# Optimization experiments

Measured on AMD Instinct MI355X. Metric: run time of the kernel, lower is better.

The kernel has to match this reference:

```python
import jax, jax.numpy as jnp
import numpy as np

B, N_FEAT, SEQ, E, H, V = 32, 196, 64, 1024, 1024, 32000


def setup_inputs() -> dict:
    key = jax.random.key(0)
    ks = jax.random.split(key, 16)
    s = 0.02
    return {
        "features": jax.random.normal(ks[0], (B, N_FEAT, E), jnp.float32),
        "captions": jax.random.randint(ks[1], (B, SEQ), 0, V),
        "max_seq_length": SEQ,
        # decoder embedding table (vocab, embed)
        "emb": jax.random.normal(ks[2], (V, E), jnp.float32) * s,
        # attention MLP: Linear(E->H), Tanh, Linear(H->1)
        "Wa1": jax.random.normal(ks[3], (H, E), jnp.float32) * s,
        "ba1": jnp.zeros((H,), jnp.float32),
        "Wa2": jax.random.normal(ks[4], (1, H), jnp.float32) * s,
        "ba2": jnp.zeros((1,), jnp.float32),
        # GRU (1 layer), input = concat(word_emb, context) -> E + H
        "W_ih": jax.random.normal(ks[5], (3 * H, E + H), jnp.float32) * s,
        "W_hh": jax.random.normal(ks[6], (3 * H, H), jnp.float32) * s,
        "b_ih": jnp.zeros((3 * H,), jnp.float32),
        "b_hh": jnp.zeros((3 * H,), jnp.float32),
        # output projection Linear(H -> V)
        "W_fc": jax.random.normal(ks[7], (V, H), jnp.float32) * s,
        "b_fc": jnp.zeros((V,), jnp.float32),
    }


def reference(features, captions, max_seq_length, emb, Wa1, ba1, Wa2, ba2,
              W_ih, W_hh, b_ih, b_hh, W_fc, b_fc):
    # words: (B, S, E)
    words = emb[captions]
    # combined: (B, N_FEAT + S, E)
    combined = jnp.concatenate([features, words], axis=1)
    # attention scores over the combined tokens, softmax along token axis
    scores = jnp.tanh(combined @ Wa1.T + ba1) @ Wa2.T + ba2   # (B, M, 1)
    A = jax.nn.softmax(scores, axis=1)                         # (B, M, 1)
    # context h0 = A^T @ combined -> (B, E); used both as GRU h0 and per-step context
    h0 = jnp.sum(A * combined, axis=1)
    context = h0

    def gru_cell(x, h):
        gi = x @ W_ih.T + b_ih          # (B, 3H)
        gh = h @ W_hh.T + b_hh          # (B, 3H)
        ir, iz, inn = jnp.split(gi, 3, axis=-1)
        hr, hz, hn = jnp.split(gh, 3, axis=-1)
        r = jax.nn.sigmoid(ir + hr)
        z = jax.nn.sigmoid(iz + hz)
        n = jnp.tanh(inn + r * hn)
        return (1.0 - z) * n + z * h

    def step(carry, _):
        input_word, h = carry
        x = jnp.concatenate([emb[input_word], context], axis=-1)  # (B, E+H)
        h_new = gru_cell(x, h)
        out = h_new @ W_fc.T + b_fc                               # (B, V)
        # greedy feedback (eval path / no teacher forcing)
        next_word = jnp.argmax(out, axis=-1)
        return (next_word, h_new), out

    init = (captions[:, 0], h0)
    (_, _), outs = jax.lax.scan(step, init, None, length=max_seq_length - 1)
    outs = jnp.transpose(outs, (1, 0, 2))                         # (B, S-1, V)
    bsz = captions.shape[0]
    vocab = W_fc.shape[0]
    outputs = jnp.concatenate(
        [jnp.zeros((bsz, 1, vocab), outs.dtype), outs], axis=1)   # t=0 stays zero
    return outputs, A
```

## Files before the change

kernel.cpp:

```cpp
#include <hip/hip_runtime.h>
#include <hip/hip_bf16.h>

typedef unsigned long long ull;
typedef unsigned int uint;

#define NB 32
#define NFEAT 196
#define SEQL 64
#define ED 1024
#define HD 1024
#define VOC 32000
#define NCOMB 260
#define NROWS (NB*NCOMB)
#define NTILE 2000
#define LBLK (NTILE/4)

typedef __attribute__((ext_vector_type(8))) short s16x8;
typedef __attribute__((ext_vector_type(4))) float f32x4;
typedef __attribute__((ext_vector_type(4))) uint  u32x4;

union FragU { u32x4 u; s16x8 s; };

#define DOT4(acc, wv, xv) acc = fmaf((wv).x,(xv).x, fmaf((wv).y,(xv).y, fmaf((wv).z,(xv).z, fmaf((wv).w,(xv).w,(acc)))))

__device__ __forceinline__ uint enc_f32(float f) {
    uint u = __float_as_uint(f);
    return (u & 0x80000000u) ? ~u : (u | 0x80000000u);
}
__device__ __forceinline__ ull shflxor64(ull v, int m) {
    uint lo = __shfl_xor((uint)v, m);
    uint hi = __shfl_xor((uint)(v >> 32), m);
    return (((ull)hi) << 32) | (ull)lo;
}

__device__ __forceinline__ void split2(float a, float b, uint& hi, uint& lo) {
    __hip_bfloat162 h2 = __float22bfloat162_rn(make_float2(a, b));
    float2 hf = __bfloat1622float2(h2);
    __hip_bfloat162 l2 = __float22bfloat162_rn(make_float2(a - hf.x, b - hf.y));
    hi = *(uint*)&h2;
    lo = *(uint*)&l2;
}

__device__ __forceinline__ void nt_store4(float* p, float a, float b, float c, float d) {
    f32x4 v = {a, b, c, d};
    __builtin_nontemporal_store(v, (f32x4*)p);
}

__device__ __forceinline__ void gh_body(
    int j, const float* __restrict__ W_hh, const float* __restrict__ h,
    float* __restrict__ gh, int w, int l)
{
    const int b0 = w*8;
    float a[3][8];
#pragma unroll
    for (int g = 0; g < 3; ++g)
#pragma unroll
        for (int i = 0; i < 8; ++i) a[g][i] = 0.f;

    const float* Ur = W_hh + (size_t)j*HD;
    const float* Uz = W_hh + (size_t)(HD + j)*HD;
    const float* Un = W_hh + (size_t)(2*HD + j)*HD;
#pragma unroll
    for (int q = 0; q < 4; ++q) {
        const int k = q*256 + l*4;
        const float4 ur = *(const float4*)(Ur + k);
        const float4 uz = *(const float4*)(Uz + k);
        const float4 un = *(const float4*)(Un + k);
#pragma unroll
        for (int i = 0; i < 8; ++i) {
            const float4 hv = *(const float4*)(h + (size_t)(b0+i)*HD + k);
            DOT4(a[0][i], ur, hv);
            DOT4(a[1][i], uz, hv);
            DOT4(a[2][i], un, hv);
        }
    }
    int s = (l >> 5) & 1;
    int ib = s*4;
    float tA[3][4];
#pragma unroll
    for (int g = 0; g < 3; ++g)
#pragma unroll
        for (int ii = 0; ii < 4; ++ii) {
            const float send = a[g][(1^s)*4 + ii];
            tA[g][ii] = a[g][s*4 + ii] + __shfl_xor(send, 32);
        }
    s = (l >> 4) & 1; ib += s*2;
    float tB[3][2];
#pragma unroll
    for (int g = 0; g < 3; ++g)
#pragma unroll
        for (int jj = 0; jj < 2; ++jj) {
            const float send = tA[g][(1^s)*2 + jj];
            tB[g][jj] = tA[g][s*2 + jj] + __shfl_xor(send, 16);
        }
    s = (l >> 3) & 1; ib += s;
    float fg[3];
#pragma unroll
    for (int g = 0; g < 3; ++g) {
        const float send = tB[g][1^s];
        fg[g] = tB[g][s] + __shfl_xor(send, 8);
    }
#pragma unroll
    for (int mm = 4; mm >= 1; mm >>= 1)
#pragma unroll
        for (int g = 0; g < 3; ++g) fg[g] += __shfl_xor(fg[g], mm);

    if ((l & 7) == 0) {
        const int b = b0 + ib;
        gh[(size_t)(0*HD + j)*NB + b] = fg[0];
        gh[(size_t)(1*HD + j)*NB + b] = fg[1];
        gh[(size_t)(2*HD + j)*NB + b] = fg[2];
    }
}

__global__ void __launch_bounds__(256) k_build(
    const float* __restrict__ features, const int* __restrict__ captions,
    const float* __restrict__ emb, float* __restrict__ combined,
    float* __restrict__ out)
{
    const int bid = blockIdx.x;
    const int t = threadIdx.x;
    if (bid < NROWS) {
        const int b = bid / NCOMB;
        const int i = bid - b*NCOMB;
        const float* src = (i < NFEAT)
            ? (features + ((size_t)(b*NFEAT + i))*ED)
            : (emb + (size_t)captions[b*SEQL + (i - NFEAT)]*ED);
        float4* dst4 = (float4*)(combined + (size_t)bid*ED);
        const float4* s4 = (const float4*)src;
        dst4[t] = s4[t];
    } else {
        const int z = bid - NROWS;
        const int m = z*1024 + t*4;
        if (m < NB*VOC) {
            const int b = m / VOC;
            const int v = m - b*VOC;
            nt_store4(out + (size_t)b*((size_t)SEQL*VOC) + v, 0.f, 0.f, 0.f, 0.f);
        }
    }
}

__global__ void __launch_bounds__(256) k_pack_w1(
    const float* __restrict__ Wa1, uint* __restrict__ W1hi, uint* __restrict__ W1lo)
{
    const int eid = blockIdx.x*256 + threadIdx.x;
    const int lane = eid & 63;
    const int ks = (eid >> 6) & 31;
    const int ct = eid >> 11;
    const int c = ct*16 + (lane & 15);
    const int k0 = ks*32 + ((lane >> 4) & 3)*4;
    const float4 wa = *(const float4*)&Wa1[(size_t)c*ED + k0];
    const float4 wb = *(const float4*)&Wa1[(size_t)c*ED + k0 + 16];
    uint hi[4], lo[4];
    split2(wa.x, wa.y, hi[0], lo[0]);
    split2(wa.z, wa.w, hi[1], lo[1]);
    split2(wb.x, wb.y, hi[2], lo[2]);
    split2(wb.z, wb.w, hi[3], lo[3]);
    *(u32x4*)&W1hi[(size_t)eid*4] = (u32x4){hi[0], hi[1], hi[2], hi[3]};
    *(u32x4*)&W1lo[(size_t)eid*4] = (u32x4){lo[0], lo[1], lo[2], lo[3]};
}

__global__ void __launch_bounds__(256) k_pack_wfc(
    const float* __restrict__ W_fc, uint* __restrict__ Whi, uint* __restrict__ Wlo)
{
    const int eid = blockIdx.x*256 + threadIdx.x;
    const int lane = eid & 63;
    const int ks = (eid >> 6) & 31;
    const int tile = eid >> 11;
    const int row = tile*16 + (lane & 15);
    const int k0 = ks*32 + ((lane >> 4) & 3)*4;
    const float4 wa = *(const float4*)&W_fc[(size_t)row*HD + k0];
    const float4 wb = *(const float4*)&W_fc[(size_t)row*HD + k0 + 16];
    uint hi[4], lo[4];
    split2(wa.x, wa.y, hi[0], lo[0]);
    split2(wa.z, wa.w, hi[1], lo[1]);
    split2(wb.x, wb.y, hi[2], lo[2]);
    split2(wb.z, wb.w, hi[3], lo[3]);
    *(u32x4*)&Whi[(size_t)eid*4] = (u32x4){hi[0], hi[1], hi[2], hi[3]};
    *(u32x4*)&Wlo[(size_t)eid*4] = (u32x4){lo[0], lo[1], lo[2], lo[3]};
}

__global__ void __launch_bounds__(256) k_attn_mfma(
    const float* __restrict__ combined, const uint* __restrict__ W1hi,
    const uint* __restrict__ W1lo, const float* __restrict__ ba1,
    const float* __restrict__ Wa2, float* __restrict__ partials)
{
    const int t = threadIdx.x;
    const int w = t >> 6, l = t & 63;
    const int lane16 = l & 15, qk = (l >> 4) & 3;
    const int rt = blockIdx.x*4 + w;
    const int cg0 = blockIdx.y*2;

    const float* Arow = combined + (size_t)(rt*16 + lane16)*ED;
    const u32x4* bh_base = (const u32x4*)W1hi + l;
    const u32x4* bl_base = (const u32x4*)W1lo + l;

    f32x4 acc[2][4];
#pragma unroll
    for (int c = 0; c < 2; ++c)
#pragma unroll
        for (int i = 0; i < 4; ++i) acc[c][i] = (f32x4){0.f,0.f,0.f,0.f};

#pragma unroll 2
    for (int ks = 0; ks < 32; ++ks) {
        const int k0 = ks*32 + qk*4;
        const float4 aa = *(const float4*)(Arow + k0);
        const float4 ab = *(const float4*)(Arow + k0 + 16);
        FragU ahi, alo;
        uint h0,l0_,h1,l1_,h2,l2_,h3,l3_;
        split2(aa.x, aa.y, h0, l0_);
        split2(aa.z, aa.w, h1, l1_);
        split2(ab.x, ab.y, h2, l2_);
        split2(ab.z, ab.w, h3, l3_);
        ahi.u = (u32x4){h0, h1, h2, h3};
        alo.u = (u32x4){l0_, l1_, l2_, l3_};
#pragma unroll
        for (int c = 0; c < 2; ++c) {
#pragma unroll
            for (int i = 0; i < 4; ++i) {
                const size_t idx = (((size_t)((cg0 + c)*4 + i))*32 + ks)*64;
                FragU bh_, bl_;
                bh_.u = bh_base[idx];
                bl_.u = bl_base[idx];
                acc[c][i] = __builtin_amdgcn_mfma_f32_16x16x32_bf16(ahi.s, bh_.s, acc[c][i], 0, 0, 0);
                acc[c][i] = __builtin_amdgcn_mfma_f32_16x16x32_bf16(ahi.s, bl_.s, acc[c][i], 0, 0, 0);
                acc[c][i] = __builtin_amdgcn_mfma_f32_16x16x32_bf16(alo.s, bh_.s, acc[c][i], 0, 0, 0);
            }
        }
    }

#pragma unroll
    for (int c = 0; c < 2; ++c) {
        const int cg = cg0 + c;
        float s[4];
#pragma unroll
        for (int r = 0; r < 4; ++r) {
            float sum = 0.f;
#pragma unroll
            for (int i = 0; i < 4; ++i) {
                const int col = cg*64 + i*16 + lane16;
                sum += tanhf(acc[c][i][r] + ba1[col]) * Wa2[col];
            }
            s[r] = sum;
        }
#pragma unroll
        for (int m = 1; m <= 8; m <<= 1)
#pragma unroll
            for (int r = 0; r < 4; ++r) s[r] += __shfl_xor(s[r], m);
        if (lane16 == 0) {
#pragma unroll
            for (int r = 0; r < 4; ++r)
                partials[(size_t)(rt*16 + qk*4 + r)*16 + cg] = s[r];
        }
    }
}

__global__ void __launch_bounds__(256) k_attn_finish(
    const float* __restrict__ partials, const float* __restrict__ combined,
    const int* __restrict__ captions,
    float* __restrict__ A_out, float* __restrict__ h0,
    float* __restrict__ ctx, ull* __restrict__ slots0)
{
    const int b = blockIdx.x, t = threadIdx.x;
    __shared__ float sc[NCOMB];
    __shared__ float red[256];

    for (int i = t; i < NCOMB; i += 256) {
        float s = 0.f;
        const float* pr = partials + (size_t)(b*NCOMB + i)*16;
#pragma unroll
        for (int g = 0; g < 16; ++g) s += pr[g];
        sc[i] = s;
    }
    __syncthreads();
    float m = -1e30f;
    for (int i = t; i < NCOMB; i += 256) m = fmaxf(m, sc[i]);
    red[t] = m; __syncthreads();
    for (int s2 = 128; s2 > 0; s2 >>= 1) {
        if (t < s2) red[t] = fmaxf(red[t], red[t+s2]);
        __syncthreads();
    }
    m = red[0]; __syncthreads();
    float ssum = 0.f;
    for (int i = t; i < NCOMB; i += 256) { float e = expf(sc[i] - m); sc[i] = e; ssum += e; }
    red[t] = ssum; __syncthreads();
    for (int s2 = 128; s2 > 0; s2 >>= 1) {
        if (t < s2) red[t] += red[t+s2];
        __syncthreads();
    }
    const float S = red[0]; __syncthreads();
    for (int i = t; i < NCOMB; i += 256) {
        const float a = sc[i] / S;
        sc[i] = a;
        A_out[b*NCOMB + i] = a;
    }
    __syncthreads();
    for (int e = t; e < HD; e += 256) {
        float acc = 0.f;
        const float* cb = combined + (size_t)b*NCOMB*ED + e;
        for (int i = 0; i < NCOMB; ++i) acc = fmaf(sc[i], cb[(size_t)i*ED], acc);
        h0[(size_t)b*HD + e] = acc;
        ctx[(size_t)b*HD + e] = acc;
    }
    if (t == 0) {
        slots0[0*NB + b] = (ull)(~(uint)captions[b*SEQL]);
#pragma unroll
        for (int g = 1; g < 8; ++g) slots0[g*NB + b] = 0ull;
    }
}

__global__ void __launch_bounds__(256) k_gictx(
    const float* __restrict__ W_ih, const float* __restrict__ b_ih,
    const float* __restrict__ ctx, float* __restrict__ gictx)
{
    const int jj = blockIdx.x;
    const int t = threadIdx.x;
    const int w = t >> 6, l = t & 63;
    const int b0 = w*8;
    const float* Wrow = W_ih + (size_t)jj*(ED+HD) + ED;

    float a[8];
#pragma unroll
    for (int i = 0; i < 8; ++i) a[i] = 0.f;
#pragma unroll
    for (int q = 0; q < 4; ++q) {
        const int k = q*256 + l*4;
        const float4 wv = *(const float4*)(Wrow + k);
#pragma unroll
        for (int i = 0; i < 8; ++i) {
            const float4 xv = *(const float4*)(ctx + (size_t)(b0 + i)*HD + k);
            DOT4(a[i], wv, xv);
        }
    }
    int s = (l >> 5) & 1;
    int ib = s*4;
    float tA[4];
#pragma unroll
    for (int ii = 0; ii < 4; ++ii) {
        const float send = a[(1^s)*4 + ii];
        tA[ii] = a[s*4 + ii] + __shfl_xor(send, 32);
    }
    s = (l >> 4) & 1; ib += s*2;
    float tB[2];
#pragma unroll
    for (int jj2 = 0; jj2 < 2; ++jj2) {
        const float send = tA[(1^s)*2 + jj2];
        tB[jj2] = tA[s*2 + jj2] + __shfl_xor(send, 16);
    }
    s = (l >> 3) & 1; ib += s;
    float fg;
    {
        const float send = tB[1^s];
        fg = tB[s] + __shfl_xor(send, 8);
    }
#pragma unroll
    for (int mm = 4; mm >= 1; mm >>= 1) fg += __shfl_xor(fg, mm);
    if ((l & 7) == 0)
        gictx[(size_t)jj*NB + (b0 + ib)] = fg + b_ih[jj];
}

__global__ void __launch_bounds__(256) k_gh(
    const float* __restrict__ W_hh, const float* __restrict__ h,
    float* __restrict__ gh)
{
    const int t = threadIdx.x;
    gh_body(blockIdx.x, W_hh, h, gh, t >> 6, t & 63);
}

__global__ void __launch_bounds__(256) k_gru_rest(
    const float* __restrict__ emb, const float* __restrict__ W_ih,
    const float* __restrict__ gh, const float* __restrict__ gictx,
    const float* __restrict__ b_hh,
    const float* __restrict__ h_prev, float* __restrict__ h_next,
    const ull* __restrict__ slots_prev, ull* __restrict__ slots_cur,
    uint* __restrict__ Hhi, uint* __restrict__ Hlo)
{
    __shared__ int word_s[NB];
    const int t = threadIdx.x;
    if (t < NB) {
        ull best = 0ull;
#pragma unroll
        for (int g = 0; g < 8; ++g) {
            ull k = slots_prev[g*NB + t];
            best = (k > best) ? k : best;
        }
        word_s[t] = (int)(~(uint)best);
    }
    if (blockIdx.x == 0) slots_cur[t] = 0ull;
    __syncthreads();

    const int j = blockIdx.x;
    const int w = t >> 6, l = t & 63;
    const int b0 = w*8;

    float a[3][8];
#pragma unroll
    for (int g = 0; g < 3; ++g)
#pragma unroll
        for (int i = 0; i < 8; ++i) a[g][i] = 0.f;

    const float* Wr = W_ih + (size_t)j*(ED+HD);
    const float* Wz = W_ih + (size_t)(HD + j)*(ED+HD);
    const float* Wn = W_ih + (size_t)(2*HD + j)*(ED+HD);
#pragma unroll
    for (int q = 0; q < 4; ++q) {
        const int k = q*256 + l*4;
        const float4 wr = *(const float4*)(Wr + k);
        const float4 wz = *(const float4*)(Wz + k);
        const float4 wn = *(const float4*)(Wn + k);
#pragma unroll
        for (int i = 0; i < 8; ++i) {
            const float4 xv = *(const float4*)(emb + (size_t)word_s[b0+i]*ED + k);
            DOT4(a[0][i], wr, xv);
            DOT4(a[1][i], wz, xv);
            DOT4(a[2][i], wn, xv);
        }
    }
    int s = (l >> 5) & 1;
    int ib = s*4;
    float tA[3][4];
#pragma unroll
    for (int g = 0; g < 3; ++g)
#pragma unroll
        for (int ii = 0; ii < 4; ++ii) {
            const float send = a[g][(1^s)*4 + ii];
            tA[g][ii] = a[g][s*4 + ii] + __shfl_xor(send, 32);
        }
    s = (l >> 4) & 1; ib += s*2;
    float tB[3][2];
#pragma unroll
    for (int g = 0; g < 3; ++g)
#pragma unroll
        for (int jj = 0; jj < 2; ++jj) {
            const float send = tA[g][(1^s)*2 + jj];
            tB[g][jj] = tA[g][s*2 + jj] + __shfl_xor(send, 16);
        }
    s = (l >> 3) & 1; ib += s;
    float fg[3];
#pragma unroll
    for (int g = 0; g < 3; ++g) {
        const float send = tB[g][1^s];
        fg[g] = tB[g][s] + __shfl_xor(send, 8);
    }
#pragma unroll
    for (int mm = 4; mm >= 1; mm >>= 1)
#pragma unroll
        for (int g = 0; g < 3; ++g) fg[g] += __shfl_xor(fg[g], mm);

    if ((l & 7) == 0) {
        const int b = b0 + ib;
        const float gcr = gictx[(size_t)j*NB + b];
        const float gcz = gictx[(size_t)(HD + j)*NB + b];
        const float gcn = gictx[(size_t)(2*HD + j)*NB + b];
        const float ghr = gh[(size_t)(0*HD + j)*NB + b];
        const float ghz = gh[(size_t)(1*HD + j)*NB + b];
        const float ghn = gh[(size_t)(2*HD + j)*NB + b];
        const float rg = 1.f/(1.f + expf(-(fg[0] + ghr + gcr + b_hh[j])));
        const float zg = 1.f/(1.f + expf(-(fg[1] + ghz + gcz + b_hh[HD+j])));
        const float ng = tanhf(fg[2] + gcn + rg*(ghn + b_hh[2*HD+j]));
        const float hp = h_prev[(size_t)b*HD + j];
        const float hv = (1.f - zg)*ng + zg*hp;
        h_next[(size_t)b*HD + j] = hv;
        __hip_bfloat16 hb = __float2bfloat16(hv);
        const float hf = __bfloat162float(hb);
        __hip_bfloat16 lb = __float2bfloat16(hv - hf);
        const int bh = b >> 4;
        const int ks = j >> 5;
        const int qk2 = (j >> 2) & 3;
        const int elem = (j & 3) + 4*((j >> 4) & 1);
        const size_t ei = (((size_t)(bh*32 + ks))*64 + qk2*16 + (b & 15))*8 + elem;
        ((ushort*)Hhi)[ei] = *(const ushort*)&hb;
        ((ushort*)Hlo)[ei] = *(const ushort*)&lb;
    }
}

__global__ void __launch_bounds__(256) k_logits_gh(
    const float* __restrict__ W_fc, const uint* __restrict__ Wfchi,
    const uint* __restrict__ Wfclo, const uint* __restrict__ Hhi,
    const uint* __restrict__ Hlo, const float* __restrict__ b_fc,
    float* __restrict__ out, ull* __restrict__ slots_cur, int tstep, int packed,
    const float* __restrict__ W_hh, const float* __restrict__ hcur,
    float* __restrict__ gh)
{
    __shared__ float sm[32][68];
    __shared__ float mergebuf[2][64][16];
    const int t = threadIdx.x;
    const int w = t >> 6, l = t & 63;

    if (blockIdx.x >= LBLK) {
        gh_body(blockIdx.x - LBLK, W_hh, hcur, gh, w, l);
        return;
    }

    const int lane16 = l & 15, qk = (l >> 4) & 3;
    const int tp = w & 1;
    const int kh = w >> 1;
    const int tile0 = blockIdx.x*4 + tp*2;

    const u32x4* hh0 = (const u32x4*)Hhi + (size_t)(kh*16)*64 + l;
    const u32x4* hl0 = (const u32x4*)Hlo + (size_t)(kh*16)*64 + l;
    const u32x4* hh1 = (const u32x4*)Hhi + (size_t)(32 + kh*16)*64 + l;
    const u32x4* hl1 = (const u32x4*)Hlo + (size_t)(32 + kh*16)*64 + l;

    f32x4 accA0 = {0.f,0.f,0.f,0.f};
    f32x4 accA1 = {0.f,0.f,0.f,0.f};
    f32x4 accB0 = {0.f,0.f,0.f,0.f};
    f32x4 accB1 = {0.f,0.f,0.f,0.f};

    if (packed) {
        const u32x4* WHa = (const u32x4*)Wfchi + ((size_t)tile0*32 + kh*16)*64 + l;
        const u32x4* WLa = (const u32x4*)Wfclo + ((size_t)tile0*32 + kh*16)*64 + l;
        const u32x4* WHb = WHa + (size_t)32*64;
        const u32x4* WLb = WLa + (size_t)32*64;
#pragma unroll 2
        for (int ks = 0; ks < 16; ++ks) {
            FragU wha, wla, whb, wlb, b0h, b0l, b1h, b1l;
            wha.u = WHa[ks*64];
            wla.u = WLa[ks*64];
            whb.u = WHb[ks*64];
            wlb.u = WLb[ks*64];
            b0h.u = hh0[ks*64];
            b0l.u = hl0[ks*64];
            b1h.u = hh1[ks*64];
            b1l.u = hl1[ks*64];
            accA0 = __builtin_amdgcn_mfma_f32_16x16x32_bf16(wha.s, b0h.s, accA0, 0, 0, 0);
            accA0 = __builtin_amdgcn_mfma_f32_16x16x32_bf16(wha.s, b0l.s, accA0, 0, 0, 0);
            accA0 = __builtin_amdgcn_mfma_f32_16x16x32_bf16(wla.s, b0h.s, accA0, 0, 0, 0);
            accA1 = __builtin_amdgcn_mfma_f32_16x16x32_bf16(wha.s, b1h.s, accA1, 0, 0, 0);
            accA1 = __builtin_amdgcn_mfma_f32_16x16x32_bf16(wha.s, b1l.s, accA1, 0, 0, 0);
            accA1 = __builtin_amdgcn_mfma_f32_16x16x32_bf16(wla.s, b1h.s, accA1, 0, 0, 0);
            accB0 = __builtin_amdgcn_mfma_f32_16x16x32_bf16(whb.s, b0h.s, accB0, 0, 0, 0);
            accB0 = __builtin_amdgcn_mfma_f32_16x16x32_bf16(whb.s, b0l.s, accB0, 0, 0, 0);
            accB0 = __builtin_amdgcn_mfma_f32_16x16x32_bf16(wlb.s, b0h.s, accB0, 0, 0, 0);
            accB1 = __builtin_amdgcn_mfma_f32_16x16x32_bf16(whb.s, b1h.s, accB1, 0, 0, 0);
            accB1 = __builtin_amdgcn_mfma_f32_16x16x32_bf16(whb.s, b1l.s, accB1, 0, 0, 0);
            accB1 = __builtin_amdgcn_mfma_f32_16x16x32_bf16(wlb.s, b1h.s, accB1, 0, 0, 0);
        }
    } else {
        const float* WrowA = W_fc + (size_t)(tile0*16 + lane16)*HD;
        const float* WrowB = W_fc + (size_t)((tile0 + 1)*16 + lane16)*HD;
#pragma unroll 2
        for (int ks = 0; ks < 16; ++ks) {
            const int k0 = (kh*16 + ks)*32 + qk*4;
            const float4 waA = *(const float4*)(WrowA + k0);
            const float4 wbA = *(const float4*)(WrowA + k0 + 16);
            const float4 waB = *(const float4*)(WrowB + k0);
            const float4 wbB = *(const float4*)(WrowB + k0 + 16);
            FragU wha, wla, whb, wlb;
            uint h0,l0_,h1,l1_,h2,l2_,h3,l3_;
            split2(waA.x, waA.y, h0, l0_);
            split2(waA.z, waA.w, h1, l1_);
            split2(wbA.x, wbA.y, h2, l2_);
            split2(wbA.z, wbA.w, h3, l3_);
            wha.u = (u32x4){h0, h1, h2, h3};
            wla.u = (u32x4){l0_, l1_, l2_, l3_};
            split2(waB.x, waB.y, h0, l0_);
            split2(waB.z, waB.w, h1, l1_);
            split2(wbB.x, wbB.y, h2, l2_);
            split2(wbB.z, wbB.w, h3, l3_);
            whb.u = (u32x4){h0, h1, h2, h3};
            wlb.u = (u32x4){l0_, l1_, l2_, l3_};
            FragU b0h, b0l, b1h, b1l;
            b0h.u = hh0[ks*64];
            b0l.u = hl0[ks*64];
            b1h.u = hh1[ks*64];
            b1l.u = hl1[ks*64];
            accA0 = __builtin_amdgcn_mfma_f32_16x16x32_bf16(wha.s, b0h.s, accA0, 0, 0, 0);
            accA0 = __builtin_amdgcn_mfma_f32_16x16x32_bf16(wha.s, b0l.s, accA0, 0, 0, 0);
            accA0 = __builtin_amdgcn_mfma_f32_16x16x32_bf16(wla.s, b0h.s, accA0, 0, 0, 0);
            accA1 = __builtin_amdgcn_mfma_f32_16x16x32_bf16(wha.s, b1h.s, accA1, 0, 0, 0);
            accA1 = __builtin_amdgcn_mfma_f32_16x16x32_bf16(wha.s, b1l.s, accA1, 0, 0, 0);
            accA1 = __builtin_amdgcn_mfma_f32_16x16x32_bf16(wla.s, b1h.s, accA1, 0, 0, 0);
            accB0 = __builtin_amdgcn_mfma_f32_16x16x32_bf16(whb.s, b0h.s, accB0, 0, 0, 0);
            accB0 = __builtin_amdgcn_mfma_f32_16x16x32_bf16(whb.s, b0l.s, accB0, 0, 0, 0);
            accB0 = __builtin_amdgcn_mfma_f32_16x16x32_bf16(wlb.s, b0h.s, accB0, 0, 0, 0);
            accB1 = __builtin_amdgcn_mfma_f32_16x16x32_bf16(whb.s, b1h.s, accB1, 0, 0, 0);
            accB1 = __builtin_amdgcn_mfma_f32_16x16x32_bf16(whb.s, b1l.s, accB1, 0, 0, 0);
            accB1 = __builtin_amdgcn_mfma_f32_16x16x32_bf16(wlb.s, b1h.s, accB1, 0, 0, 0);
        }
    }

    if (kh == 1) {
        float* rr = &mergebuf[tp][l][0];
        *(float4*)&rr[0]  = make_float4(accA0[0], accA0[1], accA0[2], accA0[3]);
        *(float4*)&rr[4]  = make_float4(accA1[0], accA1[1], accA1[2], accA1[3]);
        *(float4*)&rr[8]  = make_float4(accB0[0], accB0[1], accB0[2], accB0[3]);
        *(float4*)&rr[12] = make_float4(accB1[0], accB1[1], accB1[2], accB1[3]);
    }
    __syncthreads();
    if (kh == 0) {
        const float* rr = &mergebuf[tp][l][0];
        const float4 biasA = *(const float4*)&b_fc[tile0*16 + qk*4];
        const float4 biasB = *(const float4*)&b_fc[(tile0 + 1)*16 + qk*4];
#pragma unroll
        for (int r = 0; r < 4; ++r) {
            const int rlocA = tp*32 + qk*4 + r;
            const int rlocB = tp*32 + 16 + qk*4 + r;
            const float bA = (&biasA.x)[r];
            const float bB = (&biasB.x)[r];
            sm[lane16][rlocA]      = accA0[r] + rr[r]      + bA;
            sm[16 + lane16][rlocA] = accA1[r] + rr[4 + r]  + bA;
            sm[lane16][rlocB]      = accB0[r] + rr[8 + r]  + bB;
            sm[16 + lane16][rlocB] = accB1[r] + rr[12 + r] + bB;
        }
    }
    __syncthreads();
    {
        const int b = t >> 3;
        const int rl0 = (t & 7)*8;
        const int vbase = blockIdx.x*64 + rl0;
        float v[8];
        ull bk = 0ull;
#pragma unroll
        for (int e = 0; e < 8; ++e) {
            v[e] = sm[b][rl0 + e];
            const ull key = (((ull)enc_f32(v[e])) << 32) | (ull)(~(uint)(vbase + e));
            bk = (key > bk) ? key : bk;
        }
        float* dst = out + (size_t)b*((size_t)SEQL*VOC) + (size_t)tstep*VOC + vbase;
        nt_store4(dst,     v[0], v[1], v[2], v[3]);
        nt_store4(dst + 4, v[4], v[5], v[6], v[7]);
#pragma unroll
        for (int mm = 4; mm >= 1; mm >>= 1) {
            const ull o = shflxor64(bk, mm);
            bk = (o > bk) ? o : bk;
        }
        if ((t & 7) == 0) atomicMax(slots_cur + (blockIdx.x & 7)*NB + b, bk);
    }
}

extern "C" void kernel_launch(void* const* d_in, const int* in_sizes, int n_in,
                              void* d_out, int out_size, void* d_ws, size_t ws_size,
                              hipStream_t stream)
{
    const float* features = (const float*)d_in[0];
    const int*   captions = (const int*)d_in[1];
    const float* emb  = (const float*)d_in[3];
    const float* Wa1  = (const float*)d_in[4];
    const float* ba1  = (const float*)d_in[5];
    const float* Wa2  = (const float*)d_in[6];
    const float* W_ih = (const float*)d_in[8];
    const float* W_hh = (const float*)d_in[9];
    const float* b_ih = (const float*)d_in[10];
    const float* b_hh = (const float*)d_in[11];
    const float* W_fc = (const float*)d_in[12];
    const float* b_fc = (const float*)d_in[13];

    float* out = (float*)d_out;
    float* A_out = out + (size_t)NB*SEQL*VOC;

    char* wsp = (char*)d_ws;
    float* combined = (float*)wsp;  wsp += (size_t)NROWS*ED*4;
    float* partials = (float*)wsp;  wsp += (size_t)NROWS*16*4;
    float* hbuf0    = (float*)wsp;  wsp += (size_t)NB*HD*4;
    float* hbuf1    = (float*)wsp;  wsp += (size_t)NB*HD*4;
    float* ctx      = (float*)wsp;  wsp += (size_t)NB*HD*4;
    ull*   slots    = (ull*)wsp;    wsp += 2*8*NB*sizeof(ull);
    uint*  Hhi      = (uint*)wsp;   wsp += (size_t)4096*16;
    uint*  Hlo      = (uint*)wsp;   wsp += (size_t)4096*16;
    uint*  W1hi     = (uint*)wsp;   wsp += (size_t)131072*16;
    uint*  W1lo     = (uint*)wsp;   wsp += (size_t)131072*16;
    float* gictx    = (float*)wsp;  wsp += (size_t)3*HD*NB*4;
    float* gh       = (float*)wsp;  wsp += (size_t)3*HD*NB*4;
    uint*  Wfchi    = (uint*)wsp;   wsp += (size_t)NTILE*32*64*16;
    uint*  Wfclo    = (uint*)wsp;   wsp += (size_t)NTILE*32*64*16;
    size_t packed_need = (size_t)(wsp - (char*)d_ws);
    const int packed = (ws_size >= packed_need) ? 1 : 0;

    k_build<<<NROWS + 1000, 256, 0, stream>>>(features, captions, emb, combined, out);
    k_pack_w1<<<512, 256, 0, stream>>>(Wa1, W1hi, W1lo);
    if (packed)
        k_pack_wfc<<<NTILE*32*64/256, 256, 0, stream>>>(W_fc, Wfchi, Wfclo);
    k_attn_mfma<<<dim3(130, 8), 256, 0, stream>>>(combined, W1hi, W1lo, ba1, Wa2, partials);
    k_attn_finish<<<NB, 256, 0, stream>>>(partials, combined, captions,
                                          A_out, hbuf0, ctx, slots);
    k_gictx<<<3*HD, 256, 0, stream>>>(W_ih, b_ih, ctx, gictx);
    k_gh<<<HD, 256, 0, stream>>>(W_hh, hbuf0, gh);
    for (int t = 1; t < SEQL; ++t) {
        const float* hp = (t & 1) ? hbuf0 : hbuf1;
        float*       hn = (t & 1) ? hbuf1 : hbuf0;
        const ull* sp = slots + (size_t)((t - 1) & 1)*8*NB;
        ull*       scur = slots + (size_t)(t & 1)*8*NB;
        k_gru_rest<<<HD, 256, 0, stream>>>(emb, W_ih, gh, gictx, b_hh,
                                           hp, hn, sp, scur, Hhi, Hlo);
        k_logits_gh<<<LBLK + HD, 256, 0, stream>>>(W_fc, Wfchi, Wfclo, Hhi, Hlo,
                                                   b_fc, out, scur, t, packed,
                                                   W_hh, hn, gh);
    }
}
```

Before: 3.660 ms.

## Drop W_fc low bf16 part in logits and rescore argmax candidates in fp32

The output projection now keeps only the high bf16 half of W_fc. This removes one of the three MFMAs per tile and halves the packed weight traffic read on every decode step. Because the logits become less exact, the in-kernel argmax via atomics is replaced by a separate k_rescore kernel. That kernel collects vocab entries within a fixed margin of the row max and recomputes their dot products in fp32 to pick the greedy next word. The stored logits lose some precision. The margin and candidate cap are heuristics that could miss the true argmax, and each step now pays one more kernel launch.

```diff
diff --git a/kernel.cpp b/kernel.cpp
--- a/kernel.cpp
+++ b/kernel.cpp
@@ -14,6 +14,8 @@
 #define NROWS (NB*NCOMB)
 #define NTILE 2000
 #define LBLK (NTILE/4)
+#define RESC_MARGIN 4.0e-3f
+#define MAXCAND 32
 
 typedef __attribute__((ext_vector_type(8))) short s16x8;
 typedef __attribute__((ext_vector_type(4))) float f32x4;
@@ -26,11 +28,6 @@
 __device__ __forceinline__ uint enc_f32(float f) {
     uint u = __float_as_uint(f);
     return (u & 0x80000000u) ? ~u : (u | 0x80000000u);
-}
-__device__ __forceinline__ ull shflxor64(ull v, int m) {
-    uint lo = __shfl_xor((uint)v, m);
-    uint hi = __shfl_xor((uint)(v >> 32), m);
-    return (((ull)hi) << 32) | (ull)lo;
 }
 
 __device__ __forceinline__ void split2(float a, float b, uint& hi, uint& lo) {
@@ -39,6 +36,10 @@
     __hip_bfloat162 l2 = __float22bfloat162_rn(make_float2(a - hf.x, b - hf.y));
     hi = *(uint*)&h2;
     lo = *(uint*)&l2;
+}
+__device__ __forceinline__ uint cvt2(float a, float b) {
+    __hip_bfloat162 h2 = __float22bfloat162_rn(make_float2(a, b));
+    return *(uint*)&h2;
 }
 
 __device__ __forceinline__ void nt_store4(float* p, float a, float b, float c, float d) {
@@ -161,7 +162,7 @@
 }
 
 __global__ void __launch_bounds__(256) k_pack_wfc(
-    const float* __restrict__ W_fc, uint* __restrict__ Whi, uint* __restrict__ Wlo)
+    const float* __restrict__ W_fc, uint* __restrict__ Whi)
 {
     const int eid = blockIdx.x*256 + threadIdx.x;
     const int lane = eid & 63;
@@ -171,13 +172,8 @@
     const int k0 = ks*32 + ((lane >> 4) & 3)*4;
     const float4 wa = *(const float4*)&W_fc[(size_t)row*HD + k0];
     const float4 wb = *(const float4*)&W_fc[(size_t)row*HD + k0 + 16];
-    uint hi[4], lo[4];
-    split2(wa.x, wa.y, hi[0], lo[0]);
-    split2(wa.z, wa.w, hi[1], lo[1]);
-    split2(wb.x, wb.y, hi[2], lo[2]);
-    split2(wb.z, wb.w, hi[3], lo[3]);
-    *(u32x4*)&Whi[(size_t)eid*4] = (u32x4){hi[0], hi[1], hi[2], hi[3]};
-    *(u32x4*)&Wlo[(size_t)eid*4] = (u32x4){lo[0], lo[1], lo[2], lo[3]};
+    *(u32x4*)&Whi[(size_t)eid*4] = (u32x4){cvt2(wa.x, wa.y), cvt2(wa.z, wa.w),
+                                           cvt2(wb.x, wb.y), cvt2(wb.z, wb.w)};
 }
 
 __global__ void __launch_bounds__(256) k_attn_mfma(
@@ -259,7 +255,7 @@
     const float* __restrict__ partials, const float* __restrict__ combined,
     const int* __restrict__ captions,
     float* __restrict__ A_out, float* __restrict__ h0,
-    float* __restrict__ ctx, ull* __restrict__ slots0)
+    float* __restrict__ ctx, int* __restrict__ words)
 {
     const int b = blockIdx.x, t = threadIdx.x;
     __shared__ float sc[NCOMB];
@@ -302,11 +298,7 @@
         h0[(size_t)b*HD + e] = acc;
         ctx[(size_t)b*HD + e] = acc;
     }
-    if (t == 0) {
-        slots0[0*NB + b] = (ull)(~(uint)captions[b*SEQL]);
-#pragma unroll
-        for (int g = 1; g < 8; ++g) slots0[g*NB + b] = 0ull;
-    }
+    if (t == 0) words[b] = captions[b*SEQL];
 }
 
 __global__ void __launch_bounds__(256) k_gictx(
@@ -372,21 +364,12 @@
     const float* __restrict__ gh, const float* __restrict__ gictx,
     const float* __restrict__ b_hh,
     const float* __restrict__ h_prev, float* __restrict__ h_next,
-    const ull* __restrict__ slots_prev, ull* __restrict__ slots_cur,
+    const int* __restrict__ words,
     uint* __restrict__ Hhi, uint* __restrict__ Hlo)
 {
     __shared__ int word_s[NB];
     const int t = threadIdx.x;
-    if (t < NB) {
-        ull best = 0ull;
-#pragma unroll
-        for (int g = 0; g < 8; ++g) {
-            ull k = slots_prev[g*NB + t];
-            best = (k > best) ? k : best;
-        }
-        word_s[t] = (int)(~(uint)best);
-    }
-    if (blockIdx.x == 0) slots_cur[t] = 0ull;
+    if (t < NB) word_s[t] = words[t];
     __syncthreads();
 
     const int j = blockIdx.x;
@@ -476,11 +459,10 @@
 
 __global__ void __launch_bounds__(256) k_logits_gh(
     const float* __restrict__ W_fc, const uint* __restrict__ Wfchi,
-    const uint* __restrict__ Wfclo, const uint* __restrict__ Hhi,
-    const uint* __restrict__ Hlo, const float* __restrict__ b_fc,
-    float* __restrict__ out, ull* __restrict__ slots_cur, int tstep, int packed,
-    const float* __restrict__ W_hh, const float* __restrict__ hcur,
-    float* __restrict__ gh)
+    const uint* __restrict__ Hhi, const uint* __restrict__ Hlo,
+    const float* __restrict__ b_fc, float* __restrict__ out, int tstep,
+    int packed, const float* __restrict__ W_hh,
+    const float* __restrict__ hcur, float* __restrict__ gh)
 {
     __shared__ float sm[32][68];
     __shared__ float mergebuf[2][64][16];
@@ -509,32 +491,24 @@
 
     if (packed) {
         const u32x4* WHa = (const u32x4*)Wfchi + ((size_t)tile0*32 + kh*16)*64 + l;
-        const u32x4* WLa = (const u32x4*)Wfclo + ((size_t)tile0*32 + kh*16)*64 + l;
         const u32x4* WHb = WHa + (size_t)32*64;
-        const u32x4* WLb = WLa + (size_t)32*64;
 #pragma unroll 2
         for (int ks = 0; ks < 16; ++ks) {
-            FragU wha, wla, whb, wlb, b0h, b0l, b1h, b1l;
+            FragU wha, whb, b0h, b0l, b1h, b1l;
             wha.u = WHa[ks*64];
-            wla.u = WLa[ks*64];
             whb.u = WHb[ks*64];
-            wlb.u = WLb[ks*64];
             b0h.u = hh0[ks*64];
             b0l.u = hl0[ks*64];
             b1h.u = hh1[ks*64];
             b1l.u = hl1[ks*64];
             accA0 = __builtin_amdgcn_mfma_f32_16x16x32_bf16(wha.s, b0h.s, accA0, 0, 0, 0);
             accA0 = __builtin_amdgcn_mfma_f32_16x16x32_bf16(wha.s, b0l.s, accA0, 0, 0, 0);
-            accA0 = __builtin_amdgcn_mfma_f32_16x16x32_bf16(wla.s, b0h.s, accA0, 0, 0, 0);
             accA1 = __builtin_amdgcn_mfma_f32_16x16x32_bf16(wha.s, b1h.s, accA1, 0, 0, 0);
             accA1 = __builtin_amdgcn_mfma_f32_16x16x32_bf16(wha.s, b1l.s, accA1, 0, 0, 0);
-            accA1 = __builtin_amdgcn_mfma_f32_16x16x32_bf16(wla.s, b1h.s, accA1, 0, 0, 0);
             accB0 = __builtin_amdgcn_mfma_f32_16x16x32_bf16(whb.s, b0h.s, accB0, 0, 0, 0);
             accB0 = __builtin_amdgcn_mfma_f32_16x16x32_bf16(whb.s, b0l.s, accB0, 0, 0, 0);
-            accB0 = __builtin_amdgcn_mfma_f32_16x16x32_bf16(wlb.s, b0h.s, accB0, 0, 0, 0);
             accB1 = __builtin_amdgcn_mfma_f32_16x16x32_bf16(whb.s, b1h.s, accB1, 0, 0, 0);
             accB1 = __builtin_amdgcn_mfma_f32_16x16x32_bf16(whb.s, b1l.s, accB1, 0, 0, 0);
-            accB1 = __builtin_amdgcn_mfma_f32_16x16x32_bf16(wlb.s, b1h.s, accB1, 0, 0, 0);
         }
     } else {
         const float* WrowA = W_fc + (size_t)(tile0*16 + lane16)*HD;
@@ -546,20 +520,11 @@
             const float4 wbA = *(const float4*)(WrowA + k0 + 16);
             const float4 waB = *(const float4*)(WrowB + k0);
             const float4 wbB = *(const float4*)(WrowB + k0 + 16);
-            FragU wha, wla, whb, wlb;
-            uint h0,l0_,h1,l1_,h2,l2_,h3,l3_;
-            split2(waA.x, waA.y, h0, l0_);
-            split2(waA.z, waA.w, h1, l1_);
-            split2(wbA.x, wbA.y, h2, l2_);
-            split2(wbA.z, wbA.w, h3, l3_);
-            wha.u = (u32x4){h0, h1, h2, h3};
-            wla.u = (u32x4){l0_, l1_, l2_, l3_};
-            split2(waB.x, waB.y, h0, l0_);
-            split2(waB.z, waB.w, h1, l1_);
-            split2(wbB.x, wbB.y, h2, l2_);
-            split2(wbB.z, wbB.w, h3, l3_);
-            whb.u = (u32x4){h0, h1, h2, h3};
-            wlb.u = (u32x4){l0_, l1_, l2_, l3_};
+            FragU wha, whb;
+            wha.u = (u32x4){cvt2(waA.x, waA.y), cvt2(waA.z, waA.w),
+                            cvt2(wbA.x, wbA.y), cvt2(wbA.z, wbA.w)};
+            whb.u = (u32x4){cvt2(waB.x, waB.y), cvt2(waB.z, waB.w),
+                            cvt2(wbB.x, wbB.y), cvt2(wbB.z, wbB.w)};
             FragU b0h, b0l, b1h, b1l;
             b0h.u = hh0[ks*64];
             b0l.u = hl0[ks*64];
@@ -567,16 +532,12 @@
             b1l.u = hl1[ks*64];
             accA0 = __builtin_amdgcn_mfma_f32_16x16x32_bf16(wha.s, b0h.s, accA0, 0, 0, 0);
             accA0 = __builtin_amdgcn_mfma_f32_16x16x32_bf16(wha.s, b0l.s, accA0, 0, 0, 0);
-            accA0 = __builtin_amdgcn_mfma_f32_16x16x32_bf16(wla.s, b0h.s, accA0, 0, 0, 0);
             accA1 = __builtin_amdgcn_mfma_f32_16x16x32_bf16(wha.s, b1h.s, accA1, 0, 0, 0);
             accA1 = __builtin_amdgcn_mfma_f32_16x16x32_bf16(wha.s, b1l.s, accA1, 0, 0, 0);
-            accA1 = __builtin_amdgcn_mfma_f32_16x16x32_bf16(wla.s, b1h.s, accA1, 0, 0, 0);
             accB0 = __builtin_amdgcn_mfma_f32_16x16x32_bf16(whb.s, b0h.s, accB0, 0, 0, 0);
             accB0 = __builtin_amdgcn_mfma_f32_16x16x32_bf16(whb.s, b0l.s, accB0, 0, 0, 0);
-            accB0 = __builtin_amdgcn_mfma_f32_16x16x32_bf16(wlb.s, b0h.s, accB0, 0, 0, 0);
             accB1 = __builtin_amdgcn_mfma_f32_16x16x32_bf16(whb.s, b1h.s, accB1, 0, 0, 0);
             accB1 = __builtin_amdgcn_mfma_f32_16x16x32_bf16(whb.s, b1l.s, accB1, 0, 0, 0);
-            accB1 = __builtin_amdgcn_mfma_f32_16x16x32_bf16(wlb.s, b1h.s, accB1, 0, 0, 0);
         }
     }
 
@@ -609,23 +570,78 @@
         const int b = t >> 3;
         const int rl0 = (t & 7)*8;
         const int vbase = blockIdx.x*64 + rl0;
-        float v[8];
-        ull bk = 0ull;
-#pragma unroll
-        for (int e = 0; e < 8; ++e) {
-            v[e] = sm[b][rl0 + e];
-            const ull key = (((ull)enc_f32(v[e])) << 32) | (ull)(~(uint)(vbase + e));
-            bk = (key > bk) ? key : bk;
-        }
         float* dst = out + (size_t)b*((size_t)SEQL*VOC) + (size_t)tstep*VOC + vbase;
-        nt_store4(dst,     v[0], v[1], v[2], v[3]);
-        nt_store4(dst + 4, v[4], v[5], v[6], v[7]);
-#pragma unroll
-        for (int mm = 4; mm >= 1; mm >>= 1) {
-            const ull o = shflxor64(bk, mm);
-            bk = (o > bk) ? o : bk;
-        }
-        if ((t & 7) == 0) atomicMax(slots_cur + (blockIdx.x & 7)*NB + b, bk);
+        nt_store4(dst,     sm[b][rl0+0], sm[b][rl0+1], sm[b][rl0+2], sm[b][rl0+3]);
+        nt_store4(dst + 4, sm[b][rl0+4], sm[b][rl0+5], sm[b][rl0+6], sm[b][rl0+7]);
+    }
+}
+
+__global__ void __launch_bounds__(256) k_rescore(
+    const float* __restrict__ out, const float* __restrict__ W_fc,
+    const float* __restrict__ b_fc, const float* __restrict__ h,
+    int* __restrict__ words, int tstep)
+{
+    const int b = blockIdx.x, t = threadIdx.x;
+    const float* row = out + (size_t)b*((size_t)SEQL*VOC) + (size_t)tstep*VOC;
+    __shared__ float red[256];
+    __shared__ int cand[MAXCAND];
+    __shared__ int ncand_s;
+    __shared__ ull wkey[4];
+
+    float m = -1e30f;
+    for (int i = t*4; i < VOC; i += 1024) {
+        const float4 v = *(const float4*)&row[i];
+        m = fmaxf(m, fmaxf(fmaxf(v.x, v.y), fmaxf(v.z, v.w)));
+    }
+    red[t] = m; __syncthreads();
+    for (int s = 128; s > 0; s >>= 1) {
+        if (t < s) red[t] = fmaxf(red[t], red[t+s]);
+        __syncthreads();
+    }
+    const float thresh = red[0] - RESC_MARGIN;
+    if (t == 0) ncand_s = 0;
+    __syncthreads();
+
+    for (int i = t*4; i < VOC; i += 1024) {
+        const float4 v = *(const float4*)&row[i];
+#pragma unroll
+        for (int e = 0; e < 4; ++e) {
+            if ((&v.x)[e] >= thresh) {
+                int slot = atomicAdd(&ncand_s, 1);
+                if (slot < MAXCAND) cand[slot] = i + e;
+            }
+        }
+    }
+    __syncthreads();
+    const int nc = (ncand_s < MAXCAND) ? ncand_s : MAXCAND;
+
+    const int w = t >> 6, l = t & 63;
+    ull bk = 0ull;
+    for (int c = w; c < nc; c += 4) {
+        const int rg = cand[c];
+        const float* wr = W_fc + (size_t)rg*HD;
+        const float* hb = h + (size_t)b*HD;
+        float acc = 0.f;
+#pragma unroll
+        for (int q = 0; q < 4; ++q) {
+            const int k = q*256 + l*4;
+            const float4 wv = *(const float4*)(wr + k);
+            const float4 hv = *(const float4*)(hb + k);
+            DOT4(acc, wv, hv);
+        }
+#pragma unroll
+        for (int mm = 32; mm >= 1; mm >>= 1) acc += __shfl_xor(acc, mm);
+        const float score = acc + b_fc[rg];
+        const ull key = (((ull)enc_f32(score)) << 32) | (ull)(~(uint)rg);
+        bk = (key > bk) ? key : bk;
+    }
+    if (l == 0) wkey[w] = bk;
+    __syncthreads();
+    if (t == 0) {
+        ull best = wkey[0];
+#pragma unroll
+        for (int i = 1; i < 4; ++i) best = (wkey[i] > best) ? wkey[i] : best;
+        words[b] = (int)(~(uint)best);
     }
 }
 
@@ -655,7 +671,7 @@
     float* hbuf0    = (float*)wsp;  wsp += (size_t)NB*HD*4;
     float* hbuf1    = (float*)wsp;  wsp += (size_t)NB*HD*4;
     float* ctx      = (float*)wsp;  wsp += (size_t)NB*HD*4;
-    ull*   slots    = (ull*)wsp;    wsp += 2*8*NB*sizeof(ull);
+    int*   words    = (int*)wsp;    wsp += 256;
     uint*  Hhi      = (uint*)wsp;   wsp += (size_t)4096*16;
     uint*  Hlo      = (uint*)wsp;   wsp += (size_t)4096*16;
     uint*  W1hi     = (uint*)wsp;   wsp += (size_t)131072*16;
@@ -663,28 +679,27 @@
     float* gictx    = (float*)wsp;  wsp += (size_t)3*HD*NB*4;
     float* gh       = (float*)wsp;  wsp += (size_t)3*HD*NB*4;
     uint*  Wfchi    = (uint*)wsp;   wsp += (size_t)NTILE*32*64*16;
-    uint*  Wfclo    = (uint*)wsp;   wsp += (size_t)NTILE*32*64*16;
     size_t packed_need = (size_t)(wsp - (char*)d_ws);
     const int packed = (ws_size >= packed_need) ? 1 : 0;
 
     k_build<<<NROWS + 1000, 256, 0, stream>>>(features, captions, emb, combined, out);
     k_pack_w1<<<512, 256, 0, stream>>>(Wa1, W1hi, W1lo);
     if (packed)
-        k_pack_wfc<<<NTILE*32*64/256, 256, 0, stream>>>(W_fc, Wfchi, Wfclo);
+        k_pack_wfc<<<NTILE*32*64/256, 256, 0, stream>>>(W_fc, Wfchi);
     k_attn_mfma<<<dim3(130, 8), 256, 0, stream>>>(combined, W1hi, W1lo, ba1, Wa2, partials);
     k_attn_finish<<<NB, 256, 0, stream>>>(partials, combined, captions,
-                                          A_out, hbuf0, ctx, slots);
+                                          A_out, hbuf0, ctx, words);
     k_gictx<<<3*HD, 256, 0, stream>>>(W_ih, b_ih, ctx, gictx);
     k_gh<<<HD, 256, 0, stream>>>(W_hh, hbuf0, gh);
     for (int t = 1; t < SEQL; ++t) {
         const float* hp = (t & 1) ? hbuf0 : hbuf1;
         float*       hn = (t & 1) ? hbuf1 : hbuf0;
-        const ull* sp = slots + (size_t)((t - 1) & 1)*8*NB;
-        ull*       scur = slots + (size_t)(t & 1)*8*NB;
         k_gru_rest<<<HD, 256, 0, stream>>>(emb, W_ih, gh, gictx, b_hh,
-                                           hp, hn, sp, scur, Hhi, Hlo);
-        k_logits_gh<<<LBLK + HD, 256, 0, stream>>>(W_fc, Wfchi, Wfclo, Hhi, Hlo,
-                                                   b_fc, out, scur, t, packed,
+                                           hp, hn, words, Hhi, Hlo);
+        k_logits_gh<<<LBLK + HD, 256, 0, stream>>>(W_fc, Wfchi, Hhi, Hlo,
+                                                   b_fc, out, t, packed,
                                                    W_hh, hn, gh);
-    }
-}
+        if (t < SEQL - 1)
+            k_rescore<<<NB, 256, 0, stream>>>(out, W_fc, b_fc, hn, words, t);
+    }
+}
```

Measured after the change: 4.329 ms. 1.18x slower.
